# Kernel tuning notes

Measured on AMD Instinct MI355X. Metric: run time of the kernel, lower is better.

## Reference

```python
import jax, jax.numpy as jnp
import numpy as np

N_NODES = 50000
N_EDGES = 800000
D_FEAT = 128
EMBED = 128
HEADS = 8
HEAD_DIM = EMBED // HEADS


def setup_inputs() -> dict:
    key = jax.random.key(0)
    ks = jax.random.split(key, 10)
    xavier = jax.nn.initializers.xavier_normal()
    return {
        "nodes": jax.random.normal(ks[0], (N_NODES, D_FEAT), jnp.float32),
        "edges": jax.random.normal(ks[1], (N_EDGES, D_FEAT), jnp.float32),
        "senders": jax.random.randint(ks[2], (N_EDGES,), 0, N_NODES, jnp.int32),
        "receivers": jax.random.randint(ks[3], (N_EDGES,), 0, N_NODES, jnp.int32),
        "Ws_k": xavier(ks[4], (D_FEAT, EMBED), jnp.float32),
        "Ws_b": jnp.zeros((EMBED,), jnp.float32),
        "Wr_k": xavier(ks[5], (D_FEAT, EMBED), jnp.float32),
        "Wr_b": jnp.zeros((EMBED,), jnp.float32),
        "We_k": xavier(ks[6], (D_FEAT, EMBED), jnp.float32),
        "We_b": jnp.zeros((EMBED,), jnp.float32),
        "a": xavier(ks[7], (HEADS, HEAD_DIM), jnp.float32),
    }


def reference(nodes, edges, senders, receivers, Ws_k, Ws_b, Wr_k, Wr_b, We_k, We_b, a):
    N = nodes.shape[0]
    E = edges.shape[0]
    H, D = a.shape
    # Node-level projections (linear, so equivalent to projecting gathered edge endpoints)
    hs = nodes @ Ws_k + Ws_b            # [N, HD]  (W_s on sent attributes)
    hr = nodes @ Wr_k + Wr_b            # [N, HD]  (W_r on received attributes)
    he = edges @ We_k + We_b            # [E, HD]  (W_e on edge attributes)
    sent = hs[senders]                  # [E, HD]
    x = jax.nn.leaky_relu(sent + hr[receivers] + he)  # default slope 0.01, as original
    xh = x.reshape(E, H, D)
    logits = jnp.sum(xh * a, axis=-1)   # [E, H]
    # segment_softmax over receivers (stable: subtract per-segment max)
    mx = jax.ops.segment_max(logits, receivers, num_segments=N)  # [N, H]
    mx = jnp.where(jnp.isfinite(mx), mx, 0.0)
    ex = jnp.exp(logits - mx[receivers])                         # [E, H]
    denom = jax.ops.segment_sum(ex, receivers, num_segments=N)   # [N, H]
    w = ex / denom[receivers]                                    # [E, H]
    msg = (w[..., None] * sent.reshape(E, H, D)).reshape(E, H * D)
    out = jax.ops.segment_sum(msg, receivers, num_segments=N)    # [N, HD]
    return out
```

## Files before the change

### kernel.cpp

```cpp
#include <hip/hip_runtime.h>

#define N_NODES 50000
#define N_EDGES 800000
#define D 128
#define HEADS 8

typedef __attribute__((ext_vector_type(8))) short short8b;
typedef __attribute__((ext_vector_type(4))) float f32x4;

__device__ __forceinline__ unsigned short f2bf_rne(float f) {
    unsigned int u = __float_as_uint(f);
    u += 0x7FFFu + ((u >> 16) & 1u);
    return (unsigned short)(u >> 16);
}
__device__ __forceinline__ float bf2f(unsigned short u) {
    return __uint_as_float(((unsigned int)u) << 16);
}

#define K1_ROWS 256
__global__ __launch_bounds__(256, 3) void k_node_proj_mfma(
    const float* __restrict__ nodes,
    const float* __restrict__ Ws, const float* __restrict__ bs,
    const float* __restrict__ Wr, const float* __restrict__ br,
    unsigned short* __restrict__ hsb, unsigned short* __restrict__ hrb)
{
    __shared__ __align__(16) unsigned short WT[D][136];
    __shared__ __align__(16) unsigned short At[64][136];
    const int ntiles = (N_NODES + K1_ROWS - 1) / K1_ROWS;
    int bx = blockIdx.x;
    int proj = (bx >= ntiles) ? 1 : 0;
    int tile = proj ? (bx - ntiles) : bx;
    const float* W    = proj ? Wr : Ws;
    const float* bias = proj ? br : bs;
    unsigned short* outp = proj ? hrb : hsb;
    int t = threadIdx.x;
    int lane = t & 63;
    int wv = t >> 6;
    int lg = lane >> 4;
    int li = lane & 15;

    #pragma unroll 8
    for (int j = 0; j < 64; ++j) {
        int idx = t + 256 * j;
        int k = idx >> 7, c = idx & 127;
        WT[c][k] = f2bf_rne(W[idx]);
    }
    float b_ct[8];
    #pragma unroll
    for (int ct = 0; ct < 8; ++ct) b_ct[ct] = bias[ct * 16 + li];

    #pragma unroll 1
    for (int sub = 0; sub < 4; ++sub) {
        int row0 = tile * K1_ROWS + sub * 64;
        if (row0 >= N_NODES) break;
        __syncthreads();
        {
            const float4* Nv = (const float4*)nodes;
            #pragma unroll
            for (int j = 0; j < 8; ++j) {
                int fi = t + 256 * j;
                int r = row0 + (fi >> 5);
                float4 v = make_float4(0.f, 0.f, 0.f, 0.f);
                if (r < N_NODES) v = Nv[(size_t)r * 32 + (fi & 31)];
                ushort4 b;
                b.x = f2bf_rne(v.x); b.y = f2bf_rne(v.y);
                b.z = f2bf_rne(v.z); b.w = f2bf_rne(v.w);
                *(ushort4*)&At[fi >> 5][(fi & 31) * 4] = b;
            }
        }
        __syncthreads();

        short8b afr[4];
        #pragma unroll
        for (int kb = 0; kb < 4; ++kb)
            afr[kb] = *(const short8b*)&At[wv * 16 + li][kb * 32 + lg * 8];

        #pragma unroll
        for (int ct = 0; ct < 8; ++ct) {
            f32x4 acc = {0.f, 0.f, 0.f, 0.f};
            #pragma unroll
            for (int kb = 0; kb < 4; ++kb) {
                short8b bfr = *(const short8b*)&WT[ct * 16 + li][kb * 32 + lg * 8];
                acc = __builtin_amdgcn_mfma_f32_16x16x32_bf16(afr[kb], bfr, acc, 0, 0, 0);
            }
            #pragma unroll
            for (int j = 0; j < 4; ++j) {
                int r = row0 + wv * 16 + lg * 4 + j;
                if (r < N_NODES)
                    outp[(size_t)r * D + ct * 16 + li] = f2bf_rne(acc[j] + b_ct[ct]);
            }
        }
    }
}

#define BLK_E 64
__global__ __launch_bounds__(256, 3) void k_edge_logits_mfma(
    const float* __restrict__ edges,
    const int* __restrict__ senders, const int* __restrict__ receivers,
    const float* __restrict__ We, const float* __restrict__ be,
    const float* __restrict__ a,
    const unsigned short* __restrict__ hsb, const unsigned short* __restrict__ hrb,
    float* __restrict__ ex)
{
    __shared__ __align__(16) unsigned short WeT[D][136];
    __shared__ __align__(16) unsigned short Et[BLK_E][136];
    int t = threadIdx.x;
    int lane = t & 63;
    int wv = t >> 6;
    int lg = lane >> 4;
    int li = lane & 15;

    #pragma unroll 8
    for (int j = 0; j < 64; ++j) {
        int idx = t + 256 * j;
        int k = idx >> 7, c = idx & 127;
        WeT[c][k] = f2bf_rne(We[idx]);
    }
    float a_h[HEADS], be_h[HEADS];
    #pragma unroll
    for (int h = 0; h < HEADS; ++h) {
        a_h[h]  = a[h * 16 + li];
        be_h[h] = be[h * 16 + li];
    }
    int jm = li & 3;

    const int ntiles = N_EDGES / BLK_E;
    for (int tile = blockIdx.x; tile < ntiles; tile += gridDim.x) {
        int e0 = tile * BLK_E;

        int sj[4], rj[4];
        #pragma unroll
        for (int j = 0; j < 4; ++j) {
            int er = e0 + wv * 16 + lg * 4 + j;
            sj[j] = senders[er];
            rj[j] = receivers[er];
        }

        __syncthreads();
        {
            const float4* Ev = (const float4*)(edges + (size_t)e0 * D);
            #pragma unroll
            for (int j = 0; j < 8; ++j) {
                int fi = t + 256 * j;
                float4 v = Ev[fi];
                ushort4 b;
                b.x = f2bf_rne(v.x); b.y = f2bf_rne(v.y);
                b.z = f2bf_rne(v.z); b.w = f2bf_rne(v.w);
                *(ushort4*)&Et[fi >> 5][(fi & 31) * 4] = b;
            }
        }

        unsigned short g_hs[4][HEADS], g_hr[4][HEADS];
        #pragma unroll
        for (int j = 0; j < 4; ++j) {
            const unsigned short* hsrow = hsb + (size_t)sj[j] * D + li;
            const unsigned short* hrrow = hrb + (size_t)rj[j] * D + li;
            #pragma unroll
            for (int h = 0; h < HEADS; ++h) {
                g_hs[j][h] = hsrow[h * 16];
                g_hr[j][h] = hrrow[h * 16];
            }
        }

        __syncthreads();

        short8b afr[4];
        int erow = wv * 16 + li;
        #pragma unroll
        for (int kb = 0; kb < 4; ++kb)
            afr[kb] = *(const short8b*)&Et[erow][kb * 32 + lg * 8];

        #pragma unroll
        for (int h = 0; h < HEADS; ++h) {
            f32x4 acc = {0.f, 0.f, 0.f, 0.f};
            #pragma unroll
            for (int kb = 0; kb < 4; ++kb) {
                short8b bfr = *(const short8b*)&WeT[h * 16 + li][kb * 32 + lg * 8];
                acc = __builtin_amdgcn_mfma_f32_16x16x32_bf16(afr[kb], bfr, acc, 0, 0, 0);
            }
            float p[4];
            #pragma unroll
            for (int j = 0; j < 4; ++j) {
                float x = acc[j] + be_h[h] + bf2f(g_hs[j][h]) + bf2f(g_hr[j][h]);
                x = x > 0.f ? x : 0.01f * x;
                p[j] = x * a_h[h];
            }
            #pragma unroll
            for (int j = 0; j < 4; ++j) {
                p[j] += __shfl_xor(p[j], 1);
                p[j] += __shfl_xor(p[j], 2);
            }
            float q = (jm & 1) ? ((jm & 2) ? p[3] : p[1])
                               : ((jm & 2) ? p[2] : p[0]);
            q += __shfl_xor(q, 4);
            q += __shfl_xor(q, 8);
            float e_ = __expf(q);
            if (li < 4) {
                int er = e0 + wv * 16 + lg * 4 + li;
                ex[(size_t)er * HEADS + h] = e_;
            }
        }
    }
}

__global__ __launch_bounds__(256) void k_hist(
    const int* __restrict__ receivers, int* __restrict__ deg)
{
    int i = blockIdx.x * 256 + threadIdx.x;
    if (i < N_EDGES) atomicAdd(&deg[receivers[i]], 1);
}

#define SCAN_CHUNK 49
__global__ __launch_bounds__(1024) void k_scan(
    const int* __restrict__ deg, int* __restrict__ rowptr, int* __restrict__ cursor)
{
    __shared__ int sm[1024];
    int t = threadIdx.x;
    int base = t * SCAN_CHUNK;
    int lsum = 0;
    #pragma unroll 4
    for (int i = 0; i < SCAN_CHUNK; ++i) {
        int idx = base + i;
        if (idx < N_NODES) lsum += deg[idx];
    }
    sm[t] = lsum;
    __syncthreads();
    for (int off = 1; off < 1024; off <<= 1) {
        int v = (t >= off) ? sm[t - off] : 0;
        __syncthreads();
        sm[t] += v;
        __syncthreads();
    }
    int run = (t > 0) ? sm[t - 1] : 0;
    for (int i = 0; i < SCAN_CHUNK; ++i) {
        int idx = base + i;
        if (idx < N_NODES) {
            rowptr[idx] = run;
            cursor[idx] = run;
            run += deg[idx];
        }
    }
    if (t == 1023) rowptr[N_NODES] = sm[1023];
}

__global__ __launch_bounds__(256) void k_fill(
    const int* __restrict__ receivers, int* __restrict__ cursor,
    int* __restrict__ eids)
{
    int i = blockIdx.x * 256 + threadIdx.x;
    if (i < N_EDGES) {
        int r = receivers[i];
        int pos = atomicAdd(&cursor[r], 1);
        eids[pos] = i;
    }
}

__global__ __launch_bounds__(256) void k_gather_out(
    const int* __restrict__ rowptr, const int* __restrict__ eids,
    const int* __restrict__ senders,
    const unsigned short* __restrict__ hsb, const float* __restrict__ ex,
    float* __restrict__ out)
{
    int r = blockIdx.x * 4 + (threadIdx.x >> 6);
    int l = threadIdx.x & 63;
    int h = l >> 3;
    int beg = rowptr[r], end = rowptr[r + 1];

    float2 acc = make_float2(0.f, 0.f);
    float dsum = 0.f;
    for (int j0 = beg; j0 < end; j0 += 8) {
        int cnt = end - j0;
        int e[8], s[8]; float w[8];
        #pragma unroll
        for (int q = 0; q < 8; ++q)
            if (q < cnt) e[q] = eids[j0 + q];
        #pragma unroll
        for (int q = 0; q < 8; ++q)
            if (q < cnt) { s[q] = senders[e[q]]; w[q] = ex[(size_t)e[q] * HEADS + h]; }
        #pragma unroll
        for (int q = 0; q < 8; ++q)
            if (q < cnt) {
                ushort2 hv = *(const ushort2*)&hsb[(size_t)s[q] * D + 2 * l];
                acc.x += w[q] * bf2f(hv.x);
                acc.y += w[q] * bf2f(hv.y);
                dsum  += w[q];
            }
    }
    float inv = (end > beg && dsum != 0.f) ? (1.0f / dsum) : 0.f;
    acc.x *= inv; acc.y *= inv;
    *(float2*)&out[(size_t)r * D + 2 * l] = acc;
}

extern "C" void kernel_launch(void* const* d_in, const int* in_sizes, int n_in,
                              void* d_out, int out_size, void* d_ws, size_t ws_size,
                              hipStream_t stream) {
    const float* nodes     = (const float*)d_in[0];
    const float* edges     = (const float*)d_in[1];
    const int*   senders   = (const int*)d_in[2];
    const int*   receivers = (const int*)d_in[3];
    const float* Ws = (const float*)d_in[4];
    const float* bs = (const float*)d_in[5];
    const float* Wr = (const float*)d_in[6];
    const float* br = (const float*)d_in[7];
    const float* We = (const float*)d_in[8];
    const float* be = (const float*)d_in[9];
    const float* a  = (const float*)d_in[10];
    float* out = (float*)d_out;

    unsigned short* hsb = (unsigned short*)d_ws;
    unsigned short* hrb = hsb + (size_t)N_NODES * D;
    float* ex   = (float*)(hrb + (size_t)N_NODES * D);
    int* deg    = (int*)(ex + (size_t)N_EDGES * HEADS);
    int* rowptr = deg + N_NODES;
    int* cursor = rowptr + N_NODES + 1;
    int* eids   = cursor + N_NODES;

    int ntiles_n = (N_NODES + K1_ROWS - 1) / K1_ROWS;
    k_node_proj_mfma<<<ntiles_n * 2, 256, 0, stream>>>(nodes, Ws, bs, Wr, br, hsb, hrb);
    k_edge_logits_mfma<<<2048, 256, 0, stream>>>(edges, senders, receivers, We, be, a,
                                                 hsb, hrb, ex);
    hipMemsetAsync(deg, 0, N_NODES * sizeof(int), stream);
    k_hist<<<N_EDGES / 256, 256, 0, stream>>>(receivers, deg);
    k_scan<<<1, 1024, 0, stream>>>(deg, rowptr, cursor);
    k_fill<<<N_EDGES / 256, 256, 0, stream>>>(receivers, cursor, eids);
    k_gather_out<<<N_NODES / 4, 256, 0, stream>>>(rowptr, eids, senders, hsb, ex, out);
}
```

Baseline: 486.9 us.

## Build CSR first and compute edge logits in receiver-sorted order

The CSR build now runs before the edge kernel and also writes sender and receiver arrays permuted into receiver order. The edge-logit kernel walks edges in CSR order, gathering edge rows through eids, and writes exp-logits at CSR positions. The gather kernel then reads senders and weights contiguously instead of through two levels of indirection. In exchange, edge-feature reads become row gathers rather than a contiguous stream, and the fill kernel writes two extra index arrays.

```diff
diff --git a/kernel.cpp b/kernel.cpp
--- a/kernel.cpp
+++ b/kernel.cpp
@@ -93,116 +93,6 @@
     }
 }
 
-#define BLK_E 64
-__global__ __launch_bounds__(256, 3) void k_edge_logits_mfma(
-    const float* __restrict__ edges,
-    const int* __restrict__ senders, const int* __restrict__ receivers,
-    const float* __restrict__ We, const float* __restrict__ be,
-    const float* __restrict__ a,
-    const unsigned short* __restrict__ hsb, const unsigned short* __restrict__ hrb,
-    float* __restrict__ ex)
-{
-    __shared__ __align__(16) unsigned short WeT[D][136];
-    __shared__ __align__(16) unsigned short Et[BLK_E][136];
-    int t = threadIdx.x;
-    int lane = t & 63;
-    int wv = t >> 6;
-    int lg = lane >> 4;
-    int li = lane & 15;
-
-    #pragma unroll 8
-    for (int j = 0; j < 64; ++j) {
-        int idx = t + 256 * j;
-        int k = idx >> 7, c = idx & 127;
-        WeT[c][k] = f2bf_rne(We[idx]);
-    }
-    float a_h[HEADS], be_h[HEADS];
-    #pragma unroll
-    for (int h = 0; h < HEADS; ++h) {
-        a_h[h]  = a[h * 16 + li];
-        be_h[h] = be[h * 16 + li];
-    }
-    int jm = li & 3;
-
-    const int ntiles = N_EDGES / BLK_E;
-    for (int tile = blockIdx.x; tile < ntiles; tile += gridDim.x) {
-        int e0 = tile * BLK_E;
-
-        int sj[4], rj[4];
-        #pragma unroll
-        for (int j = 0; j < 4; ++j) {
-            int er = e0 + wv * 16 + lg * 4 + j;
-            sj[j] = senders[er];
-            rj[j] = receivers[er];
-        }
-
-        __syncthreads();
-        {
-            const float4* Ev = (const float4*)(edges + (size_t)e0 * D);
-            #pragma unroll
-            for (int j = 0; j < 8; ++j) {
-                int fi = t + 256 * j;
-                float4 v = Ev[fi];
-                ushort4 b;
-                b.x = f2bf_rne(v.x); b.y = f2bf_rne(v.y);
-                b.z = f2bf_rne(v.z); b.w = f2bf_rne(v.w);
-                *(ushort4*)&Et[fi >> 5][(fi & 31) * 4] = b;
-            }
-        }
-
-        unsigned short g_hs[4][HEADS], g_hr[4][HEADS];
-        #pragma unroll
-        for (int j = 0; j < 4; ++j) {
-            const unsigned short* hsrow = hsb + (size_t)sj[j] * D + li;
-            const unsigned short* hrrow = hrb + (size_t)rj[j] * D + li;
-            #pragma unroll
-            for (int h = 0; h < HEADS; ++h) {
-                g_hs[j][h] = hsrow[h * 16];
-                g_hr[j][h] = hrrow[h * 16];
-            }
-        }
-
-        __syncthreads();
-
-        short8b afr[4];
-        int erow = wv * 16 + li;
-        #pragma unroll
-        for (int kb = 0; kb < 4; ++kb)
-            afr[kb] = *(const short8b*)&Et[erow][kb * 32 + lg * 8];
-
-        #pragma unroll
-        for (int h = 0; h < HEADS; ++h) {
-            f32x4 acc = {0.f, 0.f, 0.f, 0.f};
-            #pragma unroll
-            for (int kb = 0; kb < 4; ++kb) {
-                short8b bfr = *(const short8b*)&WeT[h * 16 + li][kb * 32 + lg * 8];
-                acc = __builtin_amdgcn_mfma_f32_16x16x32_bf16(afr[kb], bfr, acc, 0, 0, 0);
-            }
-            float p[4];
-            #pragma unroll
-            for (int j = 0; j < 4; ++j) {
-                float x = acc[j] + be_h[h] + bf2f(g_hs[j][h]) + bf2f(g_hr[j][h]);
-                x = x > 0.f ? x : 0.01f * x;
-                p[j] = x * a_h[h];
-            }
-            #pragma unroll
-            for (int j = 0; j < 4; ++j) {
-                p[j] += __shfl_xor(p[j], 1);
-                p[j] += __shfl_xor(p[j], 2);
-            }
-            float q = (jm & 1) ? ((jm & 2) ? p[3] : p[1])
-                               : ((jm & 2) ? p[2] : p[0]);
-            q += __shfl_xor(q, 4);
-            q += __shfl_xor(q, 8);
-            float e_ = __expf(q);
-            if (li < 4) {
-                int er = e0 + wv * 16 + lg * 4 + li;
-                ex[(size_t)er * HEADS + h] = e_;
-            }
-        }
-    }
-}
-
 __global__ __launch_bounds__(256) void k_hist(
     const int* __restrict__ receivers, int* __restrict__ deg)
 {
@@ -244,20 +134,134 @@
 }
 
 __global__ __launch_bounds__(256) void k_fill(
-    const int* __restrict__ receivers, int* __restrict__ cursor,
-    int* __restrict__ eids)
+    const int* __restrict__ receivers, const int* __restrict__ senders,
+    int* __restrict__ cursor,
+    int* __restrict__ eids, int* __restrict__ s_csr, int* __restrict__ r_csr)
 {
     int i = blockIdx.x * 256 + threadIdx.x;
     if (i < N_EDGES) {
         int r = receivers[i];
         int pos = atomicAdd(&cursor[r], 1);
-        eids[pos] = i;
+        eids[pos]  = i;
+        s_csr[pos] = senders[i];
+        r_csr[pos] = r;
+    }
+}
+
+#define BLK_E 64
+__global__ __launch_bounds__(256, 3) void k_edge_logits_mfma(
+    const float* __restrict__ edges,
+    const int* __restrict__ eids, const int* __restrict__ s_csr,
+    const int* __restrict__ r_csr,
+    const float* __restrict__ We, const float* __restrict__ be,
+    const float* __restrict__ a,
+    const unsigned short* __restrict__ hsb, const unsigned short* __restrict__ hrb,
+    float* __restrict__ ex)
+{
+    __shared__ __align__(16) unsigned short WeT[D][136];
+    __shared__ __align__(16) unsigned short Et[BLK_E][136];
+    int t = threadIdx.x;
+    int lane = t & 63;
+    int wv = t >> 6;
+    int lg = lane >> 4;
+    int li = lane & 15;
+
+    #pragma unroll 8
+    for (int j = 0; j < 64; ++j) {
+        int idx = t + 256 * j;
+        int k = idx >> 7, c = idx & 127;
+        WeT[c][k] = f2bf_rne(We[idx]);
+    }
+    float a_h[HEADS], be_h[HEADS];
+    #pragma unroll
+    for (int h = 0; h < HEADS; ++h) {
+        a_h[h]  = a[h * 16 + li];
+        be_h[h] = be[h * 16 + li];
+    }
+    int jm = li & 3;
+
+    const int ntiles = N_EDGES / BLK_E;
+    for (int tile = blockIdx.x; tile < ntiles; tile += gridDim.x) {
+        int p0 = tile * BLK_E;
+
+        int sj[4], rj[4];
+        #pragma unroll
+        for (int j = 0; j < 4; ++j) {
+            int pos = p0 + wv * 16 + lg * 4 + j;
+            sj[j] = s_csr[pos];
+            rj[j] = r_csr[pos];
+        }
+
+        __syncthreads();
+        {
+            const float4* Ev = (const float4*)edges;
+            #pragma unroll
+            for (int j = 0; j < 8; ++j) {
+                int fi = t + 256 * j;
+                int e = eids[p0 + (fi >> 5)];
+                float4 v = Ev[(size_t)e * 32 + (fi & 31)];
+                ushort4 b;
+                b.x = f2bf_rne(v.x); b.y = f2bf_rne(v.y);
+                b.z = f2bf_rne(v.z); b.w = f2bf_rne(v.w);
+                *(ushort4*)&Et[fi >> 5][(fi & 31) * 4] = b;
+            }
+        }
+
+        unsigned short g_hs[4][HEADS], g_hr[4][HEADS];
+        #pragma unroll
+        for (int j = 0; j < 4; ++j) {
+            const unsigned short* hsrow = hsb + (size_t)sj[j] * D + li;
+            const unsigned short* hrrow = hrb + (size_t)rj[j] * D + li;
+            #pragma unroll
+            for (int h = 0; h < HEADS; ++h) {
+                g_hs[j][h] = hsrow[h * 16];
+                g_hr[j][h] = hrrow[h * 16];
+            }
+        }
+
+        __syncthreads();
+
+        short8b afr[4];
+        int erow = wv * 16 + li;
+        #pragma unroll
+        for (int kb = 0; kb < 4; ++kb)
+            afr[kb] = *(const short8b*)&Et[erow][kb * 32 + lg * 8];
+
+        #pragma unroll
+        for (int h = 0; h < HEADS; ++h) {
+            f32x4 acc = {0.f, 0.f, 0.f, 0.f};
+            #pragma unroll
+            for (int kb = 0; kb < 4; ++kb) {
+                short8b bfr = *(const short8b*)&WeT[h * 16 + li][kb * 32 + lg * 8];
+                acc = __builtin_amdgcn_mfma_f32_16x16x32_bf16(afr[kb], bfr, acc, 0, 0, 0);
+            }
+            float p[4];
+            #pragma unroll
+            for (int j = 0; j < 4; ++j) {
+                float x = acc[j] + be_h[h] + bf2f(g_hs[j][h]) + bf2f(g_hr[j][h]);
+                x = x > 0.f ? x : 0.01f * x;
+                p[j] = x * a_h[h];
+            }
+            #pragma unroll
+            for (int j = 0; j < 4; ++j) {
+                p[j] += __shfl_xor(p[j], 1);
+                p[j] += __shfl_xor(p[j], 2);
+            }
+            float q = (jm & 1) ? ((jm & 2) ? p[3] : p[1])
+                               : ((jm & 2) ? p[2] : p[0]);
+            q += __shfl_xor(q, 4);
+            q += __shfl_xor(q, 8);
+            float e_ = __expf(q);
+            if (li < 4) {
+                int pos = p0 + wv * 16 + lg * 4 + li;
+                ex[(size_t)pos * HEADS + h] = e_;
+            }
+        }
     }
 }
 
 __global__ __launch_bounds__(256) void k_gather_out(
-    const int* __restrict__ rowptr, const int* __restrict__ eids,
-    const int* __restrict__ senders,
+    const int* __restrict__ rowptr, const int* __restrict__ s_csr,
     const unsigned short* __restrict__ hsb, const float* __restrict__ ex,
     float* __restrict__ out)
 {
@@ -270,13 +274,10 @@
     float dsum = 0.f;
     for (int j0 = beg; j0 < end; j0 += 8) {
         int cnt = end - j0;
-        int e[8], s[8]; float w[8];
+        int s[8]; float w[8];
         #pragma unroll
         for (int q = 0; q < 8; ++q)
-            if (q < cnt) e[q] = eids[j0 + q];
-        #pragma unroll
-        for (int q = 0; q < 8; ++q)
-            if (q < cnt) { s[q] = senders[e[q]]; w[q] = ex[(size_t)e[q] * HEADS + h]; }
+            if (q < cnt) { s[q] = s_csr[j0 + q]; w[q] = ex[(size_t)(j0 + q) * HEADS + h]; }
         #pragma unroll
         for (int q = 0; q < 8; ++q)
             if (q < cnt) {
@@ -314,14 +315,17 @@
     int* rowptr = deg + N_NODES;
     int* cursor = rowptr + N_NODES + 1;
     int* eids   = cursor + N_NODES;
-
-    int ntiles_n = (N_NODES + K1_ROWS - 1) / K1_ROWS;
-    k_node_proj_mfma<<<ntiles_n * 2, 256, 0, stream>>>(nodes, Ws, bs, Wr, br, hsb, hrb);
-    k_edge_logits_mfma<<<2048, 256, 0, stream>>>(edges, senders, receivers, We, be, a,
-                                                 hsb, hrb, ex);
+    int* s_csr  = eids + N_EDGES;
+    int* r_csr  = s_csr + N_EDGES;
+
     hipMemsetAsync(deg, 0, N_NODES * sizeof(int), stream);
     k_hist<<<N_EDGES / 256, 256, 0, stream>>>(receivers, deg);
     k_scan<<<1, 1024, 0, stream>>>(deg, rowptr, cursor);
-    k_fill<<<N_EDGES / 256, 256, 0, stream>>>(receivers, cursor, eids);
-    k_gather_out<<<N_NODES / 4, 256, 0, stream>>>(rowptr, eids, senders, hsb, ex, out);
-}
+    k_fill<<<N_EDGES / 256, 256, 0, stream>>>(receivers, senders, cursor,
+                                              eids, s_csr, r_csr);
+    int ntiles_n = (N_NODES + K1_ROWS - 1) / K1_ROWS;
+    k_node_proj_mfma<<<ntiles_n * 2, 256, 0, stream>>>(nodes, Ws, bs, Wr, br, hsb, hrb);
+    k_edge_logits_mfma<<<2048, 256, 0, stream>>>(edges, eids, s_csr, r_csr,
+                                                 We, be, a, hsb, hrb, ex);
+    k_gather_out<<<N_NODES / 4, 256, 0, stream>>>(rowptr, s_csr, hsb, ex, out);
+}
```

Result: faster. 463.2 us (-4.9%).
